# Optimization experiments

Hardware: AMD Instinct MI355X
Metric: run time of the kernel (lower is better)

Reference implementation:

```python
import jax, jax.numpy as jnp
import numpy as np
import math

L, DIN, DZ, H, C, NQ, NP = 768, 384, 128, 12, 16, 4, 6
C_SQU = 1.0 / math.sqrt(C)            # scalar qk scale
W_C = math.sqrt(2.0 / (9 * NQ))       # point-distance scale


def _w(key, fan_in, fan_out):
    return jax.random.normal(key, (fan_in, fan_out), dtype=jnp.float32) / math.sqrt(fan_in)


def setup_inputs() -> dict:
    key = jax.random.key(0)
    ks = jax.random.split(key, 20)
    inp = {
        "s": jax.random.normal(ks[0], (L, DIN), dtype=jnp.float32),
        "z": jax.random.normal(ks[1], (L, L, DZ), dtype=jnp.float32),
        "rot": jax.random.normal(ks[2], (L, 3, 3), dtype=jnp.float32),
        "trans": jax.random.normal(ks[3], (L, 3), dtype=jnp.float32),
        "Wq1": _w(ks[4], DIN, H * C),
        "Wk1": _w(ks[5], DIN, H * C),
        "Wv1": _w(ks[6], DIN, H * C),
        "Wq2": _w(ks[7], DIN, H * NQ * 3),
        "Wk2": _w(ks[8], DIN, H * NQ * 3),
        "Wv3": _w(ks[9], DIN, H * NP * 3),
        "Wz": _w(ks[10], DZ, H),
        "W1": _w(ks[11], H * DZ, DIN),
        "b1": jnp.zeros((DIN,), dtype=jnp.float32),
        "W2": _w(ks[12], H * C, DIN),
        "b2": jnp.zeros((DIN,), dtype=jnp.float32),
        "W3": _w(ks[13], H * NP * 3, DIN),
        "b3": jnp.zeros((DIN,), dtype=jnp.float32),
        "gamma": jnp.zeros((H,), dtype=jnp.float32),
    }
    return inp


def ipa_transform(x, rot, trans):
    # x: [L,H,P,3] local points -> global: rot @ x + trans
    return jnp.einsum('lij,lhpj->lhpi', rot, x) + trans[:, None, None, :]


def ipa_inverse_transform(x, rot, trans):
    # global -> local: rot^T @ (x - trans)
    return jnp.einsum('lji,lhpj->lhpi', rot, x - trans[:, None, None, :])


def reference(s, z, rot, trans, Wq1, Wk1, Wv1, Wq2, Wk2, Wv3, Wz,
              W1, b1, W2, b2, W3, b3, gamma):
    q1 = (s @ Wq1).reshape(L, H, C)
    k1 = (s @ Wk1).reshape(L, H, C)
    v1 = (s @ Wv1).reshape(L, H, C)
    att = jnp.einsum('ihc,jhc->ijh', q1, k1) * C_SQU          # [L,L,H]
    bias_z = z @ Wz                                           # [L,L,H]
    q2 = ipa_transform((s @ Wq2).reshape(L, H, NQ, 3), rot, trans)
    k2 = ipa_transform((s @ Wk2).reshape(L, H, NQ, 3), rot, trans)
    # squared-distance map sum over query points & xyz, via |q|^2+|k|^2-2qk
    sq = jnp.sum(q2 * q2, axis=(-2, -1))                      # [L,H]
    sk = jnp.sum(k2 * k2, axis=(-2, -1))                      # [L,H]
    cross = jnp.einsum('ihqt,jhqt->ijh', q2, k2)              # [L,L,H]
    dismap = sq[:, None, :] + sk[None, :, :] - 2.0 * cross
    # NOTE: no softmax in the original module — raw scores weight the values.
    att = att + bias_z - jax.nn.softplus(gamma)[None, None, :] * dismap * (W_C * 0.5)
    o1 = jnp.einsum('ijh,ijd->ihd', att, z)                   # [L,H,DZ]
    o2 = jnp.einsum('jhc,ijh->ihc', v1, att)                  # [L,H,C]
    v3 = ipa_transform((s @ Wv3).reshape(L, H, NP, 3), rot, trans)
    o3 = ipa_inverse_transform(jnp.einsum('jhpt,ijh->ihpt', v3, att), rot, trans)
    out = (o1.reshape(L, -1) @ W1 + b1) \
        + (o2.reshape(L, -1) @ W2 + b2) \
        + (o3.reshape(L, -1) @ W3 + b3)
    return out
```

## Files before the change

### kernel.cpp

```cpp
#include <hip/hip_runtime.h>
#include <math.h>
#include <stdint.h>

#define LL 768
#define DIN 384
#define HH 12
#define NLIN 1080
#define WC_HALF 0.11785113019775792f
#define C_SQU 0.25f

#define OFF_LIN    0u
#define OFF_V1P    829440u
#define OFF_V3P    903168u
#define OFF_QBH    986112u
#define OFF_QBL    1133568u
#define OFF_KBH    1281024u
#define OFF_KBL    1428480u
#define OFF_WZ     1575936u
#define OFF_SQWH   1576960u
#define OFF_SKWH   1586176u
#define OFF_SX     1595392u
#define OFF_O1     8673280u
#define OFF_O2     9852928u
#define OFF_O3     10000384u

typedef __attribute__((ext_vector_type(8))) short short8v;
typedef __attribute__((ext_vector_type(4))) float float4v;

__device__ __forceinline__ ushort f2bu(float f) {
    union { float f; uint32_t u; } v; v.f = f;
    uint32_t r = (v.u + 0x7FFFu + ((v.u >> 16) & 1u)) >> 16;
    return (ushort)r;
}
__device__ __forceinline__ float bu2f(ushort u) {
    union { uint32_t u; float f; } v; v.u = ((uint32_t)u) << 16; return v.f;
}
__device__ __forceinline__ float blo2f(uint32_t u) {
    union { uint32_t u; float f; } v; v.u = u << 16; return v.f;
}
__device__ __forceinline__ float bhi2f(uint32_t u) {
    union { uint32_t u; float f; } v; v.u = u & 0xFFFF0000u; return v.f;
}

__global__ __launch_bounds__(256) void gemm_lin_kernel(
    const float* __restrict__ s,
    const float* __restrict__ Wq1, const float* __restrict__ Wk1,
    const float* __restrict__ Wv1, const float* __restrict__ Wq2,
    const float* __restrict__ Wk2, const float* __restrict__ Wv3,
    float* __restrict__ lin)
{
    const int n0 = blockIdx.x * 64;
    const int i0 = blockIdx.y * 64;
    const int tid = threadIdx.x;
    __shared__ float sT[64][17];
    __shared__ float wT[16][65];
    const int tc = tid & 15, tr = tid >> 4;
    float acc[4][4] = {};
    for (int k0 = 0; k0 < DIN; k0 += 16) {
        __syncthreads();
        for (int idx = tid; idx < 1024; idx += 256) {
            int r = idx >> 4, kk = idx & 15;
            sT[r][kk] = s[(size_t)(i0 + r) * DIN + k0 + kk];
        }
        for (int idx = tid; idx < 1024; idx += 256) {
            int kk = idx >> 6, c = idx & 63;
            int col = n0 + c;
            float v = 0.f;
            if (col < NLIN) {
                const float* W; int nout, cc2;
                if      (col < 192) { W = Wq1; nout = 192; cc2 = col; }
                else if (col < 384) { W = Wk1; nout = 192; cc2 = col - 192; }
                else if (col < 576) { W = Wv1; nout = 192; cc2 = col - 384; }
                else if (col < 720) { W = Wq2; nout = 144; cc2 = col - 576; }
                else if (col < 864) { W = Wk2; nout = 144; cc2 = col - 720; }
                else                { W = Wv3; nout = 216; cc2 = col - 864; }
                v = W[(size_t)(k0 + kk) * nout + cc2];
            }
            wT[kk][c] = v;
        }
        __syncthreads();
        #pragma unroll
        for (int kk = 0; kk < 16; ++kk) {
            float a[4], b[4];
            #pragma unroll
            for (int r = 0; r < 4; ++r) a[r] = sT[tr * 4 + r][kk];
            #pragma unroll
            for (int c = 0; c < 4; ++c) b[c] = wT[kk][tc * 4 + c];
            #pragma unroll
            for (int r = 0; r < 4; ++r)
                #pragma unroll
                for (int c = 0; c < 4; ++c) acc[r][c] += a[r] * b[c];
        }
    }
    for (int r = 0; r < 4; ++r)
        for (int c = 0; c < 4; ++c) {
            int col = n0 + tc * 4 + c;
            if (col < NLIN)
                lin[(size_t)(i0 + tr * 4 + r) * NLIN + col] = acc[r][c];
        }
}

__global__ __launch_bounds__(192) void transform_kernel(
    const float* __restrict__ lin, const float* __restrict__ rot,
    const float* __restrict__ trans, const float* __restrict__ gamma,
    const float* __restrict__ Wz,
    ushort* __restrict__ v1p, ushort* __restrict__ v3p,
    ushort* __restrict__ qbh, ushort* __restrict__ qbl,
    ushort* __restrict__ kbh, ushort* __restrict__ kbl,
    ushort* __restrict__ wzpack,
    float* __restrict__ sqwh, float* __restrict__ skwh)
{
    const int l = blockIdx.x;
    const int tid = threadIdx.x;
    __shared__ float q2s[144], k2s[144], sqp[48], skp[48];
    __shared__ float whs[12];
    __shared__ float R[9], T[3];
    if (tid < 9) R[tid] = rot[l * 9 + tid];
    if (tid >= 9 && tid < 12) T[tid - 9] = trans[l * 3 + tid - 9];
    __syncthreads();
    if (tid < 48) {
        const float* x = &lin[(size_t)l * NLIN + 576 + tid * 3];
        float x0 = x[0], x1 = x[1], x2 = x[2], ss = 0.f;
        #pragma unroll
        for (int i2 = 0; i2 < 3; ++i2) {
            float v = R[i2*3+0]*x0 + R[i2*3+1]*x1 + R[i2*3+2]*x2 + T[i2];
            q2s[tid * 3 + i2] = v; ss += v * v;
        }
        sqp[tid] = ss;
    } else if (tid < 96) {
        int t2 = tid - 48;
        const float* x = &lin[(size_t)l * NLIN + 720 + t2 * 3];
        float x0 = x[0], x1 = x[1], x2 = x[2], ss = 0.f;
        #pragma unroll
        for (int i2 = 0; i2 < 3; ++i2) {
            float v = R[i2*3+0]*x0 + R[i2*3+1]*x1 + R[i2*3+2]*x2 + T[i2];
            k2s[t2 * 3 + i2] = v; ss += v * v;
        }
        skp[t2] = ss;
    } else if (tid < 168) {
        int t2 = tid - 96;
        const float* x = &lin[(size_t)l * NLIN + 864 + t2 * 3];
        float x0 = x[0], x1 = x[1], x2 = x[2];
        #pragma unroll
        for (int i2 = 0; i2 < 3; ++i2) {
            float v = R[i2*3+0]*x0 + R[i2*3+1]*x1 + R[i2*3+2]*x2 + T[i2];
            v3p[(size_t)(l >> 1) * 432 + (t2 * 3 + i2) * 2 + (l & 1)] = f2bu(v);
        }
    }
    __syncthreads();
    if (tid < 12) {
        float sq = sqp[tid*4] + sqp[tid*4+1] + sqp[tid*4+2] + sqp[tid*4+3];
        float sk = skp[tid*4] + skp[tid*4+1] + skp[tid*4+2] + skp[tid*4+3];
        float w = logf(1.0f + expf(gamma[tid])) * WC_HALF;
        whs[tid] = w;
        sqwh[l * 12 + tid] = w * sq;
        skwh[l * 12 + tid] = w * sk;
    }
    __syncthreads();
    if (tid < 192)
        v1p[(size_t)(l >> 1) * 384 + tid * 2 + (l & 1)] =
            f2bu(lin[(size_t)l * NLIN + 384 + tid]);
    for (int idx = tid; idx < 384; idx += 192) {
        int h = idx >> 5, k = idx & 31;
        float qv, kv;
        if (k < 16) {
            qv = lin[(size_t)l * NLIN + h * 16 + k];
            kv = C_SQU * lin[(size_t)l * NLIN + 192 + h * 16 + k];
        } else if (k < 28) {
            int u = k - 16;
            qv = q2s[h * 12 + u];
            kv = 2.0f * whs[h] * k2s[h * 12 + u];
        } else { qv = 0.0f; kv = 0.0f; }
        size_t base = (size_t)l * 384 + idx;
        ushort qh = f2bu(qv), kh = f2bu(kv);
        qbh[base] = qh; qbl[base] = f2bu(qv - bu2f(qh));
        kbh[base] = kh; kbl[base] = f2bu(kv - bu2f(kh));
    }
    if (l == 0) {
        for (int idx = tid; idx < 2048; idx += 192) {
            int kb = idx >> 9, lane = (idx >> 3) & 63, e = idx & 7;
            int d = kb * 32 + (lane >> 4) * 8 + e, h = lane & 15;
            wzpack[idx] = (h < 12) ? f2bu(Wz[d * 12 + h]) : (ushort)0;
        }
    }
}

__global__ __launch_bounds__(256) void sextra_kernel(
    const ushort* __restrict__ qbh, const ushort* __restrict__ qbl,
    const ushort* __restrict__ kbh, const ushort* __restrict__ kbl,
    const float* __restrict__ sqwh, const float* __restrict__ skwh,
    float* __restrict__ sx)
{
    const int tid = threadIdx.x;
    const int wv = tid >> 6, lane = tid & 63, lm = lane & 15, g = lane >> 4;
    const int i0 = blockIdx.x * 16;
    const int jb = blockIdx.y * 64 + wv * 16;
    for (int h = 0; h < 12; ++h) {
        size_t qoff = ((size_t)(i0 + lm) * 12 + h) * 32 + g * 8;
        size_t koff = ((size_t)(jb + lm) * 12 + h) * 32 + g * 8;
        short8v ah = *(const short8v*)(qbh + qoff);
        short8v al = *(const short8v*)(qbl + qoff);
        short8v bh = *(const short8v*)(kbh + koff);
        short8v bl = *(const short8v*)(kbl + koff);
        float4v c = {0.f, 0.f, 0.f, 0.f};
        c = __builtin_amdgcn_mfma_f32_16x16x32_bf16(ah, bh, c, 0, 0, 0);
        c = __builtin_amdgcn_mfma_f32_16x16x32_bf16(ah, bl, c, 0, 0, 0);
        c = __builtin_amdgcn_mfma_f32_16x16x32_bf16(al, bh, c, 0, 0, 0);
        float skv = skwh[(jb + lm) * 12 + h];
        #pragma unroll
        for (int r = 0; r < 4; ++r) {
            int ii = i0 + g * 4 + r;
            sx[((size_t)ii * 12 + h) * 768 + jb + lm] =
                c[r] - sqwh[ii * 12 + h] - skv;
        }
    }
}

__global__ __launch_bounds__(256) void attn_kernel(
    const float* __restrict__ z, const ushort* __restrict__ v1p,
    const ushort* __restrict__ v3p, const float* __restrict__ sx,
    const ushort* __restrict__ wzp,
    const float* __restrict__ rot, const float* __restrict__ trans,
    float* __restrict__ o1, float* __restrict__ o2, float* __restrict__ o3l)
{
    const int i = blockIdx.x, tid = threadIdx.x;
    const int wv = tid >> 6, lane = tid & 63, lm = lane & 15, g = lane >> 4;
    __shared__ __attribute__((aligned(16))) char zrow[2][32 * 256];
    __shared__ __attribute__((aligned(16))) char attbh[16 * 80];
    __shared__ __attribute__((aligned(16))) char attbl[16 * 80];
    __shared__ float attf[16][33];
    __shared__ float o3s[216];

    short8v wzf[4];
    #pragma unroll
    for (int kb = 0; kb < 4; ++kb)
        wzf[kb] = *(const short8v*)(wzp + (kb * 64 + lane) * 8);

    const float4* zsrc = (const float4*)(z + (size_t)i * (LL * 128));
    const int jA = wv * 16 + lm;
    const int h2 = tid >> 4;
    const int h3 = tid / 18;

    {
        float4 z0[4];
        #pragma unroll
        for (int s = 0; s < 4; ++s) z0[s] = zsrc[s * 256 + tid];
        #pragma unroll
        for (int s = 0; s < 4; ++s) {
            int k4 = s * 256 + tid, j = k4 >> 5, d0 = (k4 & 31) * 4;
            float4 v = z0[s];
            ushort b0 = f2bu(v.x), b1 = f2bu(v.y), b2 = f2bu(v.z), b3 = f2bu(v.w);
            uint32_t lo = b0 | ((uint32_t)b1 << 16), hi = b2 | ((uint32_t)b3 << 16);
            *(uint64_t*)(&zrow[0][j * 256 + ((d0 * 2) ^ ((j & 7) << 4))]) =
                (uint64_t)lo | ((uint64_t)hi << 32);
        }
    }
    float sxr[4] = {0.f, 0.f, 0.f, 0.f};
    if (wv < 2 && g < 3) {
        #pragma unroll
        for (int r = 0; r < 4; ++r)
            sxr[r] = sx[((size_t)i * 12 + g * 4 + r) * 768 + jA];
    }
    __syncthreads();

    float4v acc1[2] = {{0.f,0.f,0.f,0.f}, {0.f,0.f,0.f,0.f}};
    float acc2 = 0.f, acc3 = 0.f;
    int p = 0;

    for (int t = 0; t < 24; ++t) {
        const int j0 = t * 32;
        float4 zreg[4];
        if (t < 23) {
            #pragma unroll
            for (int s = 0; s < 4; ++s)
                zreg[s] = zsrc[(size_t)(t + 1) * 1024 + s * 256 + tid];
        }
        uint v1u[16], v3u[16];
        if (tid < 192) {
            #pragma unroll
            for (int jp = 0; jp < 16; ++jp)
                v1u[jp] = *(const uint*)(v1p + ((size_t)(t * 16 + jp)) * 384 + tid * 2);
        }
        if (tid < 216) {
            #pragma unroll
            for (int jp = 0; jp < 16; ++jp)
                v3u[jp] = *(const uint*)(v3p + ((size_t)(t * 16 + jp)) * 432 + tid * 2);
        }
        float sxn[4] = {0.f, 0.f, 0.f, 0.f};
        if (wv < 2 && g < 3 && t < 23) {
            #pragma unroll
            for (int r = 0; r < 4; ++r)
                sxn[r] = sx[((size_t)i * 12 + g * 4 + r) * 768 + j0 + 32 + jA];
        }
        if (wv < 2) {
            float4v bias = {0.f, 0.f, 0.f, 0.f};
            #pragma unroll
            for (int kb = 0; kb < 4; ++kb) {
                short8v bz = *(const short8v*)(
                    &zrow[p][jA * 256 + ((kb * 64 + g * 16) ^ ((jA & 7) << 4))]);
                bias = __builtin_amdgcn_mfma_f32_16x16x32_bf16(wzf[kb], bz, bias, 0, 0, 0);
            }
            #pragma unroll
            for (int r = 0; r < 4; ++r) {
                int h = g * 4 + r;
                float att = bias[r] + sxr[r];
                attf[h][jA] = att;
                ushort hi = f2bu(att);
                *(ushort*)(&attbh[h * 80 + jA * 2]) = hi;
                *(ushort*)(&attbl[h * 80 + jA * 2]) = f2bu(att - bu2f(hi));
            }
        }
        __syncthreads();
        {
            short8v ah = *(const short8v*)(&attbh[lm * 80 + g * 16]);
            short8v al = *(const short8v*)(&attbl[lm * 80 + g * 16]);
            #pragma unroll
            for (int q = 0; q < 2; ++q) {
                const int b = wv * 2 + q;
                short8v bf;
                #pragma unroll
                for (int e = 0; e < 8; ++e) {
                    int jj = g * 8 + e;
                    bf[e] = *(const short*)(&zrow[p][jj * 256 +
                              (((b * 16 + lm) * 2) ^ ((jj & 7) << 4))]);
                }
                acc1[q] = __builtin_amdgcn_mfma_f32_16x16x32_bf16(ah, bf, acc1[q], 0, 0, 0);
                acc1[q] = __builtin_amdgcn_mfma_f32_16x16x32_bf16(al, bf, acc1[q], 0, 0, 0);
            }
        }
        if (tid < 192) {
            #pragma unroll
            for (int jp = 0; jp < 16; ++jp) {
                uint u = v1u[jp];
                acc2 += attf[h2][2 * jp] * blo2f(u)
                      + attf[h2][2 * jp + 1] * bhi2f(u);
            }
        }
        if (tid < 216) {
            #pragma unroll
            for (int jp = 0; jp < 16; ++jp) {
                uint u = v3u[jp];
                acc3 += attf[h3][2 * jp] * blo2f(u)
                      + attf[h3][2 * jp + 1] * bhi2f(u);
            }
        }
        if (t < 23) {
            #pragma unroll
            for (int s = 0; s < 4; ++s) {
                int k4 = s * 256 + tid, j = k4 >> 5, d0 = (k4 & 31) * 4;
                float4 v = zreg[s];
                ushort b0 = f2bu(v.x), b1 = f2bu(v.y), b2 = f2bu(v.z), b3 = f2bu(v.w);
                uint32_t lo = b0 | ((uint32_t)b1 << 16), hi = b2 | ((uint32_t)b3 << 16);
                *(uint64_t*)(&zrow[p ^ 1][j * 256 + ((d0 * 2) ^ ((j & 7) << 4))]) =
                    (uint64_t)lo | ((uint64_t)hi << 32);
            }
        }
        __syncthreads();
        #pragma unroll
        for (int r = 0; r < 4; ++r) sxr[r] = sxn[r];
        p ^= 1;
    }
    if (g < 3) {
        #pragma unroll
        for (int q = 0; q < 2; ++q) {
            const int b = wv * 2 + q;
            #pragma unroll
            for (int r = 0; r < 4; ++r)
                o1[(size_t)i * 1536 + (g * 4 + r) * 128 + b * 16 + lm] = acc1[q][r];
        }
    }
    if (tid < 192) o2[(size_t)i * 192 + tid] = acc2;
    if (tid < 216) o3s[tid] = acc3;
    __syncthreads();
    if (tid < 72) {
        float x0 = o3s[tid * 3 + 0] - trans[i * 3 + 0];
        float x1 = o3s[tid * 3 + 1] - trans[i * 3 + 1];
        float x2 = o3s[tid * 3 + 2] - trans[i * 3 + 2];
        const float* R = &rot[(size_t)i * 9];
        o3l[(size_t)i * 216 + tid * 3 + 0] = R[0]*x0 + R[3]*x1 + R[6]*x2;
        o3l[(size_t)i * 216 + tid * 3 + 1] = R[1]*x0 + R[4]*x1 + R[7]*x2;
        o3l[(size_t)i * 216 + tid * 3 + 2] = R[2]*x0 + R[5]*x1 + R[8]*x2;
    }
}

#define KCH 324
__global__ __launch_bounds__(384) void proj_kernel(
    const float* __restrict__ o1, const float* __restrict__ o2,
    const float* __restrict__ o3l,
    const float* __restrict__ W1, const float* __restrict__ W2,
    const float* __restrict__ W3,
    float* __restrict__ part)
{
    const int it = blockIdx.x, kt = blockIdx.y;
    const int tid = threadIdx.x;
    const int kbeg = kt * KCH, kend = kbeg + KCH;
    __shared__ float olds[16][KCH];
    for (int idx = tid; idx < 16 * KCH; idx += 384) {
        int r = idx / KCH, kk = idx % KCH;
        int k = kbeg + kk;
        int i = it * 16 + r;
        float v;
        if (k < 1536)      v = o1[(size_t)i * 1536 + k];
        else if (k < 1728) v = o2[(size_t)i * 192 + k - 1536];
        else               v = o3l[(size_t)i * 216 + k - 1728];
        olds[r][kk] = v;
    }
    __syncthreads();
    float acc[16] = {};
    {
        int s0 = kbeg, s1 = (kend < 1536) ? kend : 1536;
        for (int k = s0; k < s1; ++k) {
            float w = W1[(size_t)k * 384 + tid];
            int kk = k - kbeg;
            #pragma unroll
            for (int r = 0; r < 16; ++r) acc[r] += olds[r][kk] * w;
        }
    }
    {
        int s0 = (kbeg > 1536) ? kbeg : 1536, s1 = (kend < 1728) ? kend : 1728;
        for (int k = s0; k < s1; ++k) {
            float w = W2[(size_t)(k - 1536) * 384 + tid];
            int kk = k - kbeg;
            #pragma unroll
            for (int r = 0; r < 16; ++r) acc[r] += olds[r][kk] * w;
        }
    }
    {
        int s0 = (kbeg > 1728) ? kbeg : 1728, s1 = kend;
        for (int k = s0; k < s1; ++k) {
            float w = W3[(size_t)(k - 1728) * 384 + tid];
            int kk = k - kbeg;
            #pragma unroll
            for (int r = 0; r < 16; ++r) acc[r] += olds[r][kk] * w;
        }
    }
    for (int r = 0; r < 16; ++r)
        part[((size_t)kt * LL + it * 16 + r) * 384 + tid] = acc[r];
}

__global__ __launch_bounds__(256) void final_kernel(
    const float* __restrict__ part,
    const float* __restrict__ b1, const float* __restrict__ b2,
    const float* __restrict__ b3, float* __restrict__ out)
{
    int idx = blockIdx.x * 256 + threadIdx.x;
    if (idx < LL * 384) {
        int n = idx % 384;
        float v = b1[n] + b2[n] + b3[n];
        #pragma unroll
        for (int kt = 0; kt < 6; ++kt) v += part[(size_t)kt * 294912 + idx];
        out[idx] = v;
    }
}

extern "C" void kernel_launch(void* const* d_in, const int* in_sizes, int n_in,
                              void* d_out, int out_size, void* d_ws, size_t ws_size,
                              hipStream_t stream) {
    const float* s     = (const float*)d_in[0];
    const float* z     = (const float*)d_in[1];
    const float* rot   = (const float*)d_in[2];
    const float* trans = (const float*)d_in[3];
    const float* Wq1   = (const float*)d_in[4];
    const float* Wk1   = (const float*)d_in[5];
    const float* Wv1   = (const float*)d_in[6];
    const float* Wq2   = (const float*)d_in[7];
    const float* Wk2   = (const float*)d_in[8];
    const float* Wv3   = (const float*)d_in[9];
    const float* Wz    = (const float*)d_in[10];
    const float* W1    = (const float*)d_in[11];
    const float* b1    = (const float*)d_in[12];
    const float* W2    = (const float*)d_in[13];
    const float* b2    = (const float*)d_in[14];
    const float* W3    = (const float*)d_in[15];
    const float* b3    = (const float*)d_in[16];
    const float* gamma = (const float*)d_in[17];
    float* ws  = (float*)d_ws;
    float* out = (float*)d_out;

    float*  lin  = ws + OFF_LIN;
    ushort* v1p  = (ushort*)(ws + OFF_V1P);
    ushort* v3p  = (ushort*)(ws + OFF_V3P);
    ushort* qbh  = (ushort*)(ws + OFF_QBH);
    ushort* qbl  = (ushort*)(ws + OFF_QBL);
    ushort* kbh  = (ushort*)(ws + OFF_KBH);
    ushort* kbl  = (ushort*)(ws + OFF_KBL);
    ushort* wzp  = (ushort*)(ws + OFF_WZ);
    float*  sqwh = ws + OFF_SQWH;
    float*  skwh = ws + OFF_SKWH;
    float*  sx   = ws + OFF_SX;
    float*  o1   = ws + OFF_O1;
    float*  o2   = ws + OFF_O2;
    float*  o3l  = ws + OFF_O3;
    float*  part = ws + OFF_SX;

    dim3 gA(17, 12);
    gemm_lin_kernel<<<gA, 256, 0, stream>>>(s, Wq1, Wk1, Wv1, Wq2, Wk2, Wv3, lin);
    transform_kernel<<<LL, 192, 0, stream>>>(lin, rot, trans, gamma, Wz,
                                             v1p, v3p, qbh, qbl, kbh, kbl, wzp,
                                             sqwh, skwh);
    dim3 gS(48, 12);
    sextra_kernel<<<gS, 256, 0, stream>>>(qbh, qbl, kbh, kbl, sqwh, skwh, sx);
    attn_kernel<<<LL, 256, 0, stream>>>(z, v1p, v3p, sx, wzp, rot, trans,
                                        o1, o2, o3l);
    dim3 gC(48, 6);
    proj_kernel<<<gC, 384, 0, stream>>>(o1, o2, o3l, W1, W2, W3, part);
    final_kernel<<<(LL * 384 + 255) / 256, 256, 0, stream>>>(part, b1, b2, b3, out);
}
```

Before: 324.1 us.

## Relayout q/k packs head-major, change z LDS swizzle, vectorize attf reads

Stores the packed q/k bf16 arrays and the sq/sk weight vectors head-major so the sextra kernel reads contiguous rows per head, and adds an unroll hint to its head loop. Changes the XOR swizzle used for the bf16 z tile in shared memory to a new pattern meant to cut bank conflicts on the transposed reads. Pads attf to 36 floats with 16-byte alignment so the v1/v3 reductions can use float4 shared-memory loads. The main risks are the new swizzle still conflicting on some access pattern and a wider padded row adding its own bank conflicts.

After: 324.4 us. No clear change (+0.1%).

```diff
diff --git a/kernel.cpp b/kernel.cpp
--- a/kernel.cpp
+++ b/kernel.cpp
@@ -40,6 +40,9 @@
 }
 __device__ __forceinline__ float bhi2f(uint32_t u) {
     union { uint32_t u; float f; } v; v.u = u & 0xFFFF0000u; return v.f;
+}
+__device__ __forceinline__ int fswz(int j) {
+    return (((j >> 3) << 1) | ((j >> 1) & 1)) << 4;
 }
 
 __global__ __launch_bounds__(256) void gemm_lin_kernel(
@@ -153,8 +156,8 @@
         float sk = skp[tid*4] + skp[tid*4+1] + skp[tid*4+2] + skp[tid*4+3];
         float w = logf(1.0f + expf(gamma[tid])) * WC_HALF;
         whs[tid] = w;
-        sqwh[l * 12 + tid] = w * sq;
-        skwh[l * 12 + tid] = w * sk;
+        sqwh[tid * 768 + l] = w * sq;
+        skwh[tid * 768 + l] = w * sk;
     }
     __syncthreads();
     if (tid < 192)
@@ -171,7 +174,7 @@
             qv = q2s[h * 12 + u];
             kv = 2.0f * whs[h] * k2s[h * 12 + u];
         } else { qv = 0.0f; kv = 0.0f; }
-        size_t base = (size_t)l * 384 + idx;
+        size_t base = ((size_t)h * 768 + l) * 32 + k;
         ushort qh = f2bu(qv), kh = f2bu(kv);
         qbh[base] = qh; qbl[base] = f2bu(qv - bu2f(qh));
         kbh[base] = kh; kbl[base] = f2bu(kv - bu2f(kh));
@@ -195,9 +198,10 @@
     const int wv = tid >> 6, lane = tid & 63, lm = lane & 15, g = lane >> 4;
     const int i0 = blockIdx.x * 16;
     const int jb = blockIdx.y * 64 + wv * 16;
+    #pragma unroll 2
     for (int h = 0; h < 12; ++h) {
-        size_t qoff = ((size_t)(i0 + lm) * 12 + h) * 32 + g * 8;
-        size_t koff = ((size_t)(jb + lm) * 12 + h) * 32 + g * 8;
+        size_t qoff = ((size_t)h * 768 + i0 + lm) * 32 + g * 8;
+        size_t koff = ((size_t)h * 768 + jb + lm) * 32 + g * 8;
         short8v ah = *(const short8v*)(qbh + qoff);
         short8v al = *(const short8v*)(qbl + qoff);
         short8v bh = *(const short8v*)(kbh + koff);
@@ -206,12 +210,12 @@
         c = __builtin_amdgcn_mfma_f32_16x16x32_bf16(ah, bh, c, 0, 0, 0);
         c = __builtin_amdgcn_mfma_f32_16x16x32_bf16(ah, bl, c, 0, 0, 0);
         c = __builtin_amdgcn_mfma_f32_16x16x32_bf16(al, bh, c, 0, 0, 0);
-        float skv = skwh[(jb + lm) * 12 + h];
+        float skv = skwh[h * 768 + jb + lm];
         #pragma unroll
         for (int r = 0; r < 4; ++r) {
             int ii = i0 + g * 4 + r;
             sx[((size_t)ii * 12 + h) * 768 + jb + lm] =
-                c[r] - sqwh[ii * 12 + h] - skv;
+                c[r] - sqwh[h * 768 + ii] - skv;
         }
     }
 }
@@ -228,7 +232,7 @@
     __shared__ __attribute__((aligned(16))) char zrow[2][32 * 256];
     __shared__ __attribute__((aligned(16))) char attbh[16 * 80];
     __shared__ __attribute__((aligned(16))) char attbl[16 * 80];
-    __shared__ float attf[16][33];
+    __shared__ __attribute__((aligned(16))) float attf[16][36];
     __shared__ float o3s[216];
 
     short8v wzf[4];
@@ -251,7 +255,7 @@
             float4 v = z0[s];
             ushort b0 = f2bu(v.x), b1 = f2bu(v.y), b2 = f2bu(v.z), b3 = f2bu(v.w);
             uint32_t lo = b0 | ((uint32_t)b1 << 16), hi = b2 | ((uint32_t)b3 << 16);
-            *(uint64_t*)(&zrow[0][j * 256 + ((d0 * 2) ^ ((j & 7) << 4))]) =
+            *(uint64_t*)(&zrow[0][j * 256 + ((d0 * 2) ^ fswz(j))]) =
                 (uint64_t)lo | ((uint64_t)hi << 32);
         }
     }
@@ -297,7 +301,7 @@
             #pragma unroll
             for (int kb = 0; kb < 4; ++kb) {
                 short8v bz = *(const short8v*)(
-                    &zrow[p][jA * 256 + ((kb * 64 + g * 16) ^ ((jA & 7) << 4))]);
+                    &zrow[p][jA * 256 + ((kb * 64 + g * 16) ^ fswz(jA))]);
                 bias = __builtin_amdgcn_mfma_f32_16x16x32_bf16(wzf[kb], bz, bias, 0, 0, 0);
             }
             #pragma unroll
@@ -322,26 +326,30 @@
                 for (int e = 0; e < 8; ++e) {
                     int jj = g * 8 + e;
                     bf[e] = *(const short*)(&zrow[p][jj * 256 +
-                              (((b * 16 + lm) * 2) ^ ((jj & 7) << 4))]);
+                              (((b * 16 + lm) * 2) ^ fswz(jj))]);
                 }
                 acc1[q] = __builtin_amdgcn_mfma_f32_16x16x32_bf16(ah, bf, acc1[q], 0, 0, 0);
                 acc1[q] = __builtin_amdgcn_mfma_f32_16x16x32_bf16(al, bf, acc1[q], 0, 0, 0);
             }
         }
         if (tid < 192) {
-            #pragma unroll
-            for (int jp = 0; jp < 16; ++jp) {
-                uint u = v1u[jp];
-                acc2 += attf[h2][2 * jp] * blo2f(u)
-                      + attf[h2][2 * jp + 1] * bhi2f(u);
+            const float4* af = (const float4*)(&attf[h2][0]);
+            #pragma unroll
+            for (int c4 = 0; c4 < 8; ++c4) {
+                float4 a = af[c4];
+                uint u0 = v1u[2 * c4], u1 = v1u[2 * c4 + 1];
+                acc2 += a.x * blo2f(u0) + a.y * bhi2f(u0)
+                      + a.z * blo2f(u1) + a.w * bhi2f(u1);
             }
         }
         if (tid < 216) {
-            #pragma unroll
-            for (int jp = 0; jp < 16; ++jp) {
-                uint u = v3u[jp];
-                acc3 += attf[h3][2 * jp] * blo2f(u)
-                      + attf[h3][2 * jp + 1] * bhi2f(u);
+            const float4* af = (const float4*)(&attf[h3][0]);
+            #pragma unroll
+            for (int c4 = 0; c4 < 8; ++c4) {
+                float4 a = af[c4];
+                uint u0 = v3u[2 * c4], u1 = v3u[2 * c4 + 1];
+                acc3 += a.x * blo2f(u0) + a.y * bhi2f(u0)
+                      + a.z * blo2f(u1) + a.w * bhi2f(u1);
             }
         }
         if (t < 23) {
@@ -351,7 +359,7 @@
                 float4 v = zreg[s];
                 ushort b0 = f2bu(v.x), b1 = f2bu(v.y), b2 = f2bu(v.z), b3 = f2bu(v.w);
                 uint32_t lo = b0 | ((uint32_t)b1 << 16), hi = b2 | ((uint32_t)b3 << 16);
-                *(uint64_t*)(&zrow[p ^ 1][j * 256 + ((d0 * 2) ^ ((j & 7) << 4))]) =
+                *(uint64_t*)(&zrow[p ^ 1][j * 256 + ((d0 * 2) ^ fswz(j))]) =
                     (uint64_t)lo | ((uint64_t)hi << 32);
             }
         }
```
